# Performance work log

Hardware: AMD Instinct MI355X
Metric: run time of the kernel (lower is better)

The kernel has to match this reference:

```python
import jax, jax.numpy as jnp
import numpy as np

EMB = 384
HID = 256
HEADS = 4
HD = HID // HEADS  # 64
LAYERS = 2
M_DOCS = 32
TOTAL = 4096  # 1 query + 32 docs + 4063 sentences
LN_EPS = 1e-5


def _layernorm(x, scale, bias):
    mu = jnp.mean(x, axis=-1, keepdims=True)
    var = jnp.mean(jnp.square(x - mu), axis=-1, keepdims=True)
    return (x - mu) * jax.lax.rsqrt(var + LN_EPS) * scale + bias


def setup_inputs() -> dict:
    key = jax.random.key(0)
    ks = jax.random.split(key, 12)
    g = 0.05  # small init scale (stand-in for xavier)
    return {
        "node_embeddings": jax.random.normal(ks[0], (TOTAL, EMB), jnp.float32),
        "adj": jax.random.randint(ks[1], (TOTAL, TOTAL), 0, 2, jnp.int32),
        "num_docs": M_DOCS,
        "proj_w": jax.random.normal(ks[2], (HID, EMB), jnp.float32) * g,
        "proj_b": jnp.zeros((HID,), jnp.float32),
        "ln_scale": jnp.ones((LAYERS, HID), jnp.float32),
        "ln_bias": jnp.zeros((LAYERS, HID), jnp.float32),
        "gat_W": jax.random.normal(ks[3], (LAYERS, HEADS, HD, HID), jnp.float32) * g,
        "gat_a": jax.random.normal(ks[4], (LAYERS, HEADS, 2 * HD), jnp.float32) * g,
        "fusion_w": jax.random.normal(ks[5], (HID, 2 * HID + 2), jnp.float32) * g,
        "fusion_b": jnp.zeros((HID,), jnp.float32),
        "out_w": jax.random.normal(ks[6], (HID,), jnp.float32) * g,
        "out_b": jnp.float32(0.5),
    }


def reference(node_embeddings, adj, num_docs, proj_w, proj_b, ln_scale, ln_bias,
              gat_W, gat_a, fusion_w, fusion_b, out_w, out_b):
    T = node_embeddings.shape[0]
    M = num_docs
    N = T - 1 - M  # number of sentences
    # input projection + relu (dropout = identity in eval)
    h = jax.nn.relu(node_embeddings @ proj_w.T + proj_b)  # (T, HID)
    # query-guided sentence re-weighting
    q = h[0:1]                     # (1, HID)
    s = h[1 + M:]                  # (N, HID)
    qn = q / (jnp.linalg.norm(q, axis=1, keepdims=True) + 1e-8)
    sn = s / (jnp.linalg.norm(s, axis=1, keepdims=True) + 1e-8)
    cos = (qn @ sn.T).reshape(-1, 1)          # (N,1)
    s = s + 0.8 * q * cos
    h = jnp.concatenate([h[:1 + M], s], axis=0)
    mask = (adj == 0)[None]                   # (1,T,T)
    for i in range(LAYERS):
        res = h
        x = _layernorm(h, ln_scale[i], ln_bias[i])
        Wh = jnp.einsum('nd,hkd->hnk', x, gat_W[i])                # (H,T,HD)
        # concat-attention a.[Wh_i ; Wh_j] == a_src.Wh_i + a_dst.Wh_j
        src = jnp.einsum('hnk,hk->hn', Wh, gat_a[i, :, :HD])       # (H,T)
        dst = jnp.einsum('hnk,hk->hn', Wh, gat_a[i, :, HD:])       # (H,T)
        e = jax.nn.leaky_relu(src[:, :, None] + dst[:, None, :], 0.2)  # (H,T,T)
        e = jnp.where(mask, -jnp.inf, e)
        attn = jax.nn.softmax(e, axis=-1)                          # softmax over j
        hn = jnp.einsum('hij,hjk->hik', attn, Wh)                  # (H,T,HD)
        hcat = jnp.transpose(hn, (1, 0, 2)).reshape(T, HEADS * HD)
        h = 0.5 * jax.nn.relu(hcat) + 0.5 * res
    qh = h[0:1]
    sh = h[1 + M:]
    scores = (qh @ sh.T) / (HID ** 0.5)       # (1,N)
    aw = jax.nn.softmax(scores, axis=-1)
    awT = aw.T                                # (N,1)
    qw = qh * (awT + 0.5)                     # (N,HID)
    qnf = qh / (jnp.linalg.norm(qh, axis=1, keepdims=True) + 1e-8)
    snf = sh / (jnp.linalg.norm(sh, axis=1, keepdims=True) + 1e-8)
    cosf = (qnf @ snf.T).reshape(-1, 1)       # (N,1)
    feat = jnp.concatenate([sh, qw, cosf, awT], axis=1)  # (N, 2*HID+2)
    g = jax.nn.relu(feat @ fusion_w.T + fusion_b)
    out = g @ out_w + out_b                   # (N,)
    return out + 0.5 * cosf[:, 0]
```

## Files before the change

### kernel.cpp

```cpp
#include <hip/hip_runtime.h>
#include <hip/hip_bf16.h>
#include <stdint.h>

#define TOTAL 4096
#define EMB 384
#define MD 32
#define NDOCS (TOTAL - 1 - MD)
#define LN_EPS 1e-5f
#define NEGF (-1e30f)

typedef __hip_bfloat16 bf16;
typedef unsigned short ushort_t;
typedef __attribute__((ext_vector_type(8))) short short8;
typedef __attribute__((ext_vector_type(4))) float f32x4;
typedef __attribute__((ext_vector_type(2))) float f32x2;

__device__ __forceinline__ float ldf(const void* p, int i, int isbf) {
    return isbf ? __bfloat162float(((const bf16*)p)[i]) : ((const float*)p)[i];
}

__device__ __forceinline__ unsigned f2bf(float x) {
    return (__float_as_uint(x) + 0x8000u) >> 16;
}

__device__ __forceinline__ unsigned fenc(float f) {
    unsigned u = __float_as_uint(f);
    return (u >> 31) ? ~u : (u | 0x80000000u);
}
__device__ __forceinline__ float fdec(unsigned k) {
    return __uint_as_float((k & 0x80000000u) ? (k & 0x7FFFFFFFu) : ~k);
}

#define NTRANS ((EMB * 256 + 2 * 65536 + 514 * 256) / 256)
__global__ void k_adjmask(const int* adj, unsigned long long* maskb,
                          const uint16_t* embp, int* flag, unsigned* dmaxu,
                          const void* proj_w, const void* gat_W, const void* fusion_w,
                          float* projT, float* gatT, float* fwT) {
    __shared__ int red[4];
    int i = blockIdx.x, t = threadIdx.x;
    int w = t >> 6, l = t & 63;
    for (int c = w; c < 64; c += 4) {
        int a = adj[(size_t)i * TOTAL + c * 64 + l];
        unsigned long long m = __ballot(a != 0);
        if (l == 0) maskb[i * 64 + c] = m;
    }
    if (i == 0) {
        for (int idx = t; idx < 2048; idx += 256) dmaxu[idx] = 0x007FFFFFu;
    }
    if (i < NTRANS) {
        int cnt = 0;
        for (int k = t; k < 4096; k += 256) {
            uint16_t wd = embp[2 * k];
            int e = (wd >> 7) & 0xFF;
            if (e >= 100 && e <= 140) cnt++;
        }
        for (int o = 32; o > 0; o >>= 1) cnt += __shfl_down(cnt, o);
        if ((t & 63) == 0) red[t >> 6] = cnt;
        __syncthreads();
        int isbf = (red[0] + red[1] + red[2] + red[3] > 2048) ? 1 : 0;
        if (i == 0 && t == 0) flag[0] = isbf;
        int idx = i * 256 + t;
        if (idx < EMB * 256) {
            int d = idx >> 8, c = idx & 255;
            projT[idx] = ldf(proj_w, c * EMB + d, isbf);
        } else if (idx < EMB * 256 + 2 * 65536) {
            int r = idx - EMB * 256;
            int ll = r >> 16, rem = r & 65535;
            int d = rem >> 8, c = rem & 255;
            gatT[r] = ldf(gat_W, ll * 65536 + c * 256 + d, isbf);
        } else {
            int r = idx - (EMB * 256 + 2 * 65536);
            int j = r >> 8, c = r & 255;
            fwT[r] = ldf(fusion_w, c * 514 + j, isbf);
        }
    }
}

#define LR 8
__global__ __launch_bounds__(512) void k_lnwh(
        const void* emb, const void* proj_b, const float* projT,
        float* h, const float* gatT, const void* ln_scale, const void* ln_bias,
        const void* gat_a, ushort_t* whswz, float* srcb, unsigned* d12g,
        unsigned* dmaxu, int layer, const int* flagp) {
    __shared__ float embs[9][EMB];
    __shared__ float xs[8][256];
    __shared__ float red[2][LR][4];
    __shared__ float qred[4];
    int isbf = flagp[0];
    int t5 = threadIdx.x;
    int t = t5 & 255, half = t5 >> 8;
    int l = t5 & 63;
    int wh = (t5 >> 6) & 3;
    int i0 = blockIdx.x * LR;
    float hv[4];
    if (layer == 0) {
        for (int idx = t5; idx < 9 * EMB; idx += 512) {
            int r = idx / EMB, d = idx % EMB;
            embs[r][d] = ldf(emb, ((r < 8) ? (i0 + r) : 0) * EMB + d, isbf);
        }
        __syncthreads();
        float bias0 = ldf(proj_b, t, isbf);
        float acc[4] = {0.f, 0.f, 0.f, 0.f};
        float qacc = 0.f;
        for (int d0 = 0; d0 < EMB; d0 += 4) {
            float w0 = projT[d0 * 256 + t];
            float w1 = projT[(d0 + 1) * 256 + t];
            float w2 = projT[(d0 + 2) * 256 + t];
            float w3 = projT[(d0 + 3) * 256 + t];
            float4 xq = *(const float4*)&embs[8][d0];
            qacc = fmaf(xq.x, w0, qacc); qacc = fmaf(xq.y, w1, qacc);
            qacc = fmaf(xq.z, w2, qacc); qacc = fmaf(xq.w, w3, qacc);
#pragma unroll
            for (int r = 0; r < 4; r++) {
                float4 x = *(const float4*)&embs[half * 4 + r][d0];
                acc[r] = fmaf(x.x, w0, acc[r]); acc[r] = fmaf(x.y, w1, acc[r]);
                acc[r] = fmaf(x.z, w2, acc[r]); acc[r] = fmaf(x.w, w3, acc[r]);
            }
        }
        float qv = fmaxf(qacc + bias0, 0.f);
#pragma unroll
        for (int r = 0; r < 4; r++) hv[r] = fmaxf(acc[r] + bias0, 0.f);
        {
            float a = qv * qv;
            for (int o = 32; o > 0; o >>= 1) a += __shfl_down(a, o);
            if (half == 0 && l == 0) qred[wh] = a;
        }
#pragma unroll
        for (int r = 0; r < 4; r++) {
            float b = hv[r] * hv[r], c = qv * hv[r];
            for (int o = 32; o > 0; o >>= 1) { b += __shfl_down(b, o); c += __shfl_down(c, o); }
            if (l == 0) { red[0][half * 4 + r][wh] = b; red[1][half * 4 + r][wh] = c; }
        }
        __syncthreads();
        if (i0 + LR > 1 + MD) {
            float qn = sqrtf(qred[0] + qred[1] + qred[2] + qred[3]) + 1e-8f;
#pragma unroll
            for (int r = 0; r < 4; r++) {
                int rr = half * 4 + r;
                int i = i0 + rr;
                if (i >= 1 + MD) {
                    float bs = red[0][rr][0] + red[0][rr][1] + red[0][rr][2] + red[0][rr][3];
                    float cs = red[1][rr][0] + red[1][rr][1] + red[1][rr][2] + red[1][rr][3];
                    float k = 0.8f * (cs / (qn * (sqrtf(bs) + 1e-8f)));
                    hv[r] += k * qv;
                }
            }
        }
#pragma unroll
        for (int r = 0; r < 4; r++)
            h[(size_t)(i0 + half * 4 + r) * 256 + t] = hv[r];
        __syncthreads();
    } else {
#pragma unroll
        for (int r = 0; r < 4; r++)
            hv[r] = h[(size_t)(i0 + half * 4 + r) * 256 + t];
    }
    float scale = ldf(ln_scale, layer * 256 + t, isbf);
    float lbias = ldf(ln_bias, layer * 256 + t, isbf);
#pragma unroll
    for (int r = 0; r < 4; r++) {
        float a = hv[r], b = hv[r] * hv[r];
        for (int o = 32; o > 0; o >>= 1) { a += __shfl_down(a, o); b += __shfl_down(b, o); }
        if (l == 0) { red[0][half * 4 + r][wh] = a; red[1][half * 4 + r][wh] = b; }
    }
    __syncthreads();
#pragma unroll
    for (int r = 0; r < 4; r++) {
        int rr = half * 4 + r;
        float mu = (red[0][rr][0] + red[0][rr][1] + red[0][rr][2] + red[0][rr][3]) * (1.f / 256.f);
        float var = (red[1][rr][0] + red[1][rr][1] + red[1][rr][2] + red[1][rr][3]) * (1.f / 256.f) - mu * mu;
        xs[rr][t] = (hv[r] - mu) * rsqrtf(var + LN_EPS) * scale + lbias;
    }
    __syncthreads();
    const float* gT = gatT + layer * 65536;
    float acc2[4] = {0.f, 0.f, 0.f, 0.f};
    for (int d0 = 0; d0 < 256; d0 += 4) {
        float w0 = gT[d0 * 256 + t];
        float w1 = gT[(d0 + 1) * 256 + t];
        float w2 = gT[(d0 + 2) * 256 + t];
        float w3 = gT[(d0 + 3) * 256 + t];
#pragma unroll
        for (int r = 0; r < 4; r++) {
            float4 x = *(const float4*)&xs[half * 4 + r][d0];
            acc2[r] = fmaf(x.x, w0, acc2[r]); acc2[r] = fmaf(x.y, w1, acc2[r]);
            acc2[r] = fmaf(x.z, w2, acc2[r]); acc2[r] = fmaf(x.w, w3, acc2[r]);
        }
    }
    float av1 = ldf(gat_a, layer * 512 + wh * 128 + l, isbf);
    float av2 = ldf(gat_a, layer * 512 + wh * 128 + 64 + l, isbf);
    const float LOG2E = 1.44269504f;
    float mmax = -__builtin_inff();
#pragma unroll
    for (int r = 0; r < 4; r++) {
        int i = i0 + half * 4 + r;
        int off = (i >> 6) * 16384 + (t >> 6) * 4096 + ((i >> 3) & 7) * 512 +
                  ((t >> 4) & 3) * 128 + (t & 15) * 8 + (i & 7);
        whswz[off] = (ushort_t)f2bf(acc2[r]);
        float sv = acc2[r] * av1, dv = acc2[r] * av2;
        for (int o = 32; o > 0; o >>= 1) { sv += __shfl_down(sv, o); dv += __shfl_down(dv, o); }
        if (l == 0) {
            srcb[wh * 4096 + i] = sv;
            float D1 = exp2f(dv * LOG2E), D2 = exp2f(0.2f * dv * LOG2E);
            d12g[wh * 4096 + i] = (f2bf(D2) << 16) | f2bf(D1);
            mmax = fmaxf(mmax, dv);
        }
    }
    if (l == 0) atomicMax(&dmaxu[(blockIdx.x & 63) * 16 + wh], fenc(mmax));
}

#define TI 16
__global__ __launch_bounds__(512) void k_pv(const ushort_t* whswz, const float* srcb,
                                            const unsigned* dmaxu, const unsigned* d12g,
                                            const unsigned long long* maskb, float* h) {
    __shared__ unsigned long long mbs[16 * 66];
    __shared__ __align__(16) f32x4 accsh[16 * 64];
    __shared__ __align__(16) float lsh[4][4][4];
    __shared__ float srcs[64];
    __shared__ float dmx[4];
    __shared__ unsigned mlut[4];
    int t = threadIdx.x;
    int W = t >> 6, lane = t & 63;
    int hH = W & 3, kq = W >> 2;
    int quad = lane >> 4, c16 = lane & 15;
    int i0 = blockIdx.x * TI;
    if (t < 4) mlut[t] = (t & 1 ? 0x0000FFFFu : 0u) | (t & 2 ? 0xFFFF0000u : 0u);
    if (t < 256) {
        int hh = t >> 6, sl = t & 63;
        float v = fdec(dmaxu[sl * 16 + hh]);
        for (int o = 32; o > 0; o >>= 1) v = fmaxf(v, __shfl_xor(v, o));
        if (sl == 0) dmx[hh] = v;
    }
    for (int idx = t; idx < 16 * 64; idx += 512) {
        int r = idx >> 6, wd = idx & 63;
        mbs[r * 66 + wd] = maskb[(size_t)(i0 + r) * 64 + wd];
    }
    if (t < 64) srcs[t] = srcb[(t >> 4) * 4096 + i0 + (t & 15)];
    __syncthreads();
    const float LOG2E = 1.44269504f;
    float dm = dmx[hH];
    float src = srcs[hH * 16 + c16];
    float sd = src + dm;
    float rce = -fmaxf(sd, 0.2f * sd);
    float E1 = exp2f((src + rce) * LOG2E);
    float E2 = exp2f((0.2f * src + rce) * LOG2E);
    f32x4 acc[4];
    f32x4 accl = (f32x4){0.f, 0.f, 0.f, 0.f};
#pragma unroll
    for (int ct = 0; ct < 4; ct++) acc[ct] = (f32x4){0.f, 0.f, 0.f, 0.f};
    uint4 onesu;
    unsigned os = (c16 == 0) ? 0x3F803F80u : 0u;
    onesu.x = os; onesu.y = os; onesu.z = os; onesu.w = os;
    short8 bfones = __builtin_bit_cast(short8, onesu);
    const uint4* g4 = (const uint4*)whswz;
    const uint4* d4 = (const uint4*)d12g;
    size_t b0 = (size_t)hH * 512 + (size_t)(kq * 4 + quad) * 64 + c16;
    int dbase = hH * 1024, d0i = kq * 8 + quad * 2;
    uint4 bn[4], dn0, dn1;
#pragma unroll
    for (int ct = 0; ct < 4; ct++) bn[ct] = g4[b0 + ct * 16];
    dn0 = d4[dbase + d0i]; dn1 = d4[dbase + d0i + 1];
    for (int step = 0; step < 64; step++) {
        uint4 bc[4];
#pragma unroll
        for (int ct = 0; ct < 4; ct++) bc[ct] = bn[ct];
        uint4 dc0 = dn0, dc1 = dn1;
        if (step < 63) {
            size_t bs = b0 + (size_t)(step + 1) * 2048;
#pragma unroll
            for (int ct = 0; ct < 4; ct++) bn[ct] = g4[bs + ct * 16];
            int di = dbase + (step + 1) * 16 + d0i;
            dn0 = d4[di]; dn1 = d4[di + 1];
        }
        unsigned mby = (unsigned)(mbs[c16 * 66 + step] >> (kq * 32 + quad * 8)) & 0xFFu;
        unsigned dw[8] = {dc0.x, dc0.y, dc0.z, dc0.w, dc1.x, dc1.y, dc1.z, dc1.w};
        unsigned pu[4];
#pragma unroll
        for (int q = 0; q < 4; q++) {
            unsigned a = dw[2 * q], b = dw[2 * q + 1];
            f32x2 D1 = (f32x2){__uint_as_float(a << 16), __uint_as_float(b << 16)};
            f32x2 D2 = (f32x2){__uint_as_float(a & 0xFFFF0000u), __uint_as_float(b & 0xFFFF0000u)};
            f32x2 v1 = D1 * E1;
            f32x2 v2 = D2 * E2;
            f32x2 m = __builtin_elementwise_max(v1, v2);
            unsigned v = ((__float_as_uint(m.x) + 0x8000u) >> 16) |
                         ((__float_as_uint(m.y) + 0x8000u) & 0xFFFF0000u);
            pu[q] = v & mlut[(mby >> (2 * q)) & 3u];
        }
        uint4 afu;
        afu.x = pu[0]; afu.y = pu[1]; afu.z = pu[2]; afu.w = pu[3];
        short8 af = __builtin_bit_cast(short8, afu);
#pragma unroll
        for (int ct = 0; ct < 4; ct++) {
            short8 bf = __builtin_bit_cast(short8, bc[ct]);
            acc[ct] = __builtin_amdgcn_mfma_f32_16x16x32_bf16(af, bf, acc[ct], 0, 0, 0);
        }
        accl = __builtin_amdgcn_mfma_f32_16x16x32_bf16(af, bfones, accl, 0, 0, 0);
    }
    __syncthreads();
    if (kq == 1) {
#pragma unroll
        for (int ct = 0; ct < 4; ct++)
            accsh[(hH * 4 + ct) * 64 + lane] = acc[ct];
        if (c16 == 0) *(f32x4*)&lsh[hH][quad][0] = accl;
    }
    __syncthreads();
    if (kq == 0) {
        float ls[4];
#pragma unroll
        for (int rr = 0; rr < 4; rr++)
            ls[rr] = __shfl(accl[rr], quad * 16) + lsh[hH][quad][rr];
#pragma unroll
        for (int ct = 0; ct < 4; ct++) {
            f32x4 o = acc[ct] + accsh[(hH * 4 + ct) * 64 + lane];
#pragma unroll
            for (int rr = 0; rr < 4; rr++) {
                int row = i0 + quad * 4 + rr;
                size_t idx = (size_t)row * 256 + hH * 64 + ct * 16 + c16;
                float hn = 0.5f * fmaxf(o[rr] / ls[rr], 0.f) + 0.5f * h[idx];
                h[idx] = hn;
            }
        }
    }
}

__global__ __launch_bounds__(256) void k_scores(const float* h, float* scoresv, float* cosv,
                                                float* swp) {
    int t = threadIdx.x, W = t >> 6, lane = t & 63;
    const float4* h4 = (const float4*)h;
    int gw = blockIdx.x * 4 + W;
    float4 q4 = h4[lane];
    float a = q4.x * q4.x + q4.y * q4.y + q4.z * q4.z + q4.w * q4.w;
    for (int o = 32; o > 0; o >>= 1) a += __shfl_xor(a, o);
    float qn = sqrtf(a) + 1e-8f;
    float mw = NEGF, sw = 0.f;
    for (int n = gw; n < NDOCS; n += 1024) {
        float4 s4 = h4[(size_t)(1 + MD + n) * 64 + lane];
        float b = s4.x * s4.x + s4.y * s4.y + s4.z * s4.z + s4.w * s4.w;
        float c = q4.x * s4.x + q4.y * s4.y + q4.z * s4.z + q4.w * s4.w;
        for (int o = 32; o > 0; o >>= 1) { b += __shfl_xor(b, o); c += __shfl_xor(c, o); }
        float sc = c * (1.f / 16.f);
        if (lane == 0) {
            scoresv[n] = sc;
            cosv[n] = c / (qn * (sqrtf(b) + 1e-8f));
        }
        float mn = fmaxf(mw, sc);
        sw = sw * __expf(mw - mn) + __expf(sc - mn);
        mw = mn;
    }
    if (lane == 0) { swp[2 * gw] = mw; swp[2 * gw + 1] = sw; }
}

#define TN 8
__global__ __launch_bounds__(256) void k_fusion(const float* h,
                                                const float* scoresv, const float* swp,
                                                const float* cosv,
                                                const float* fwT, const void* fusion_b,
                                                const void* out_w, const void* out_bp,
                                                void* outv, const int* flagp) {
    __shared__ float feats2[514][TN];
    __shared__ float qhs[256];
    __shared__ float red[TN][4];
    __shared__ float reds[2][4];
    __shared__ float aws[TN];
    int isbf = flagp[0];
    int t = threadIdx.x;
    int n0 = blockIdx.x * TN;
    qhs[t] = h[t];
    float M = NEGF, S = 0.f;
    for (int idx = t; idx < 1024; idx += 256) {
        float pm = swp[2 * idx], ps = swp[2 * idx + 1];
        float mn = fmaxf(M, pm);
        S = S * __expf(M - mn) + ps * __expf(pm - mn);
        M = mn;
    }
    for (int o = 32; o > 0; o >>= 1) {
        float m2 = __shfl_xor(M, o), s2 = __shfl_xor(S, o);
        float mn = fmaxf(M, m2);
        S = S * __expf(M - mn) + s2 * __expf(m2 - mn);
        M = mn;
    }
    if ((t & 63) == 0) { reds[0][t >> 6] = M; reds[1][t >> 6] = S; }
    __syncthreads();
    float Mf = fmaxf(fmaxf(reds[0][0], reds[0][1]), fmaxf(reds[0][2], reds[0][3]));
    float Sf = reds[1][0] * __expf(reds[0][0] - Mf) + reds[1][1] * __expf(reds[0][1] - Mf) +
               reds[1][2] * __expf(reds[0][2] - Mf) + reds[1][3] * __expf(reds[0][3] - Mf);
    float invS = 1.f / Sf;
    if (t < TN) {
        int n = n0 + t;
        aws[t] = (n < NDOCS) ? __expf(scoresv[n] - Mf) * invS : 0.f;
    }
    __syncthreads();
    for (int idx = t; idx < 514 * TN; idx += 256) {
        int j = idx >> 3, r = idx & 7;
        int n = n0 + r;
        float v = 0.f;
        if (n < NDOCS) {
            if (j < 256) v = h[(size_t)(1 + MD + n) * 256 + j];
            else if (j < 512) v = qhs[j - 256] * (aws[r] + 0.5f);
            else if (j == 512) v = cosv[n];
            else v = aws[r];
        }
        feats2[j][r] = v;
    }
    __syncthreads();
    float acc[TN];
    float bk = ldf(fusion_b, t, isbf);
#pragma unroll
    for (int r = 0; r < TN; r++) acc[r] = bk;
    for (int j0 = 0; j0 < 512; j0 += 8) {
        float wv[8];
#pragma unroll
        for (int u = 0; u < 8; u++) wv[u] = fwT[(j0 + u) * 256 + t];
#pragma unroll
        for (int u = 0; u < 8; u++) {
            float4 fa = *(const float4*)&feats2[j0 + u][0];
            float4 fb = *(const float4*)&feats2[j0 + u][4];
            acc[0] = fmaf(fa.x, wv[u], acc[0]); acc[1] = fmaf(fa.y, wv[u], acc[1]);
            acc[2] = fmaf(fa.z, wv[u], acc[2]); acc[3] = fmaf(fa.w, wv[u], acc[3]);
            acc[4] = fmaf(fb.x, wv[u], acc[4]); acc[5] = fmaf(fb.y, wv[u], acc[5]);
            acc[6] = fmaf(fb.z, wv[u], acc[6]); acc[7] = fmaf(fb.w, wv[u], acc[7]);
        }
    }
#pragma unroll
    for (int j = 512; j < 514; j++) {
        float wv = fwT[j * 256 + t];
#pragma unroll
        for (int r = 0; r < TN; r++) acc[r] = fmaf(feats2[j][r], wv, acc[r]);
    }
    float ow = ldf(out_w, t, isbf);
    float outb = ldf(out_bp, 0, isbf);
#pragma unroll
    for (int r = 0; r < TN; r++) {
        float o = fmaxf(acc[r], 0.f) * ow;
        for (int off = 32; off > 0; off >>= 1) o += __shfl_down(o, off);
        if ((t & 63) == 0) red[r][t >> 6] = o;
    }
    __syncthreads();
    if (t < TN) {
        int n = n0 + t;
        if (n < NDOCS) {
            float o = red[t][0] + red[t][1] + red[t][2] + red[t][3] + outb + 0.5f * cosv[n];
            if (isbf) ((bf16*)outv)[n] = __float2bfloat16(o);
            else      ((float*)outv)[n] = o;
        }
    }
}

extern "C" void kernel_launch(void* const* d_in, const int* in_sizes, int n_in,
                              void* d_out, int out_size, void* d_ws, size_t ws_size,
                              hipStream_t stream) {
    const void* emb      = d_in[0];
    const int*  adj      = (const int*)d_in[1];
    const void* proj_w   = d_in[3];
    const void* proj_b   = d_in[4];
    const void* ln_scale = d_in[5];
    const void* ln_bias  = d_in[6];
    const void* gat_W    = d_in[7];
    const void* gat_a    = d_in[8];
    const void* fusion_w = d_in[9];
    const void* fusion_b = d_in[10];
    const void* out_w    = d_in[11];
    const void* out_b    = d_in[12];

    unsigned long long* maskb = (unsigned long long*)d_ws;
    int* flag = (int*)((char*)d_ws + (size_t)4096 * 64 * 8);
    float* f = (float*)((char*)d_ws + (size_t)4096 * 64 * 8 + 256);
    float* h       = f; f += 4096 * 256;
    float* srcb    = f; f += 4 * 4096;
    unsigned* d12g = (unsigned*)f; f += 4 * 4096;
    unsigned* dmaxu = (unsigned*)f; f += 2048;
    float* projT   = f; f += EMB * 256;
    float* gatT    = f; f += 2 * 65536;
    float* fwT     = f; f += 514 * 256;
    float* scoresv = f; f += 4096;
    float* cosv    = f; f += 4096;
    float* swpart  = f; f += 2048;
    ushort_t* whswz = (ushort_t*)f; f += 4096 * 256 / 2;

    k_adjmask<<<dim3(4096), dim3(256), 0, stream>>>(adj, maskb, (const uint16_t*)emb, flag,
                                                    dmaxu, proj_w, gat_W, fusion_w,
                                                    projT, gatT, fwT);
    for (int layer = 0; layer < 2; layer++) {
        k_lnwh<<<dim3(TOTAL / LR), dim3(512), 0, stream>>>(emb, proj_b, projT, h, gatT,
                                                           ln_scale, ln_bias, gat_a,
                                                           whswz, srcb, d12g,
                                                           dmaxu + layer * 1024, layer, flag);
        k_pv<<<dim3(TOTAL / TI), dim3(512), 0, stream>>>(whswz, srcb, dmaxu + layer * 1024,
                                                         d12g, maskb, h);
    }
    k_scores<<<dim3(256), dim3(256), 0, stream>>>(h, scoresv, cosv, swpart);
    k_fusion<<<dim3((NDOCS + TN - 1) / TN), dim3(256), 0, stream>>>(h, scoresv, swpart,
                                                                    cosv, fwT, fusion_b, out_w,
                                                                    out_b, (void*)d_out, flag);
}
```

Before: 317.8 us.

## Interleave transposed weights for float4 loads and deepen PV prefetch pipeline

The transposed projection, GAT and fusion weight layouts are reorganised so each thread reads four consecutive k-values as one float4, and the dense matvec loops software-prefetch the next weight vector. The attention PV kernel's register prefetch goes from one step ahead to two, using two alternating register sets. These aim to cut global load instruction count and hide memory latency, at the cost of more register pressure in the MFMA loop. fwT grows slightly to hold the padded 4-wide layout.

```diff
diff --git a/kernel.cpp b/kernel.cpp
--- a/kernel.cpp
+++ b/kernel.cpp
@@ -62,16 +62,17 @@
         int idx = i * 256 + t;
         if (idx < EMB * 256) {
             int d = idx >> 8, c = idx & 255;
-            projT[idx] = ldf(proj_w, c * EMB + d, isbf);
+            projT[(d >> 2) * 1024 + c * 4 + (d & 3)] = ldf(proj_w, c * EMB + d, isbf);
         } else if (idx < EMB * 256 + 2 * 65536) {
             int r = idx - EMB * 256;
             int ll = r >> 16, rem = r & 65535;
             int d = rem >> 8, c = rem & 255;
-            gatT[r] = ldf(gat_W, ll * 65536 + c * 256 + d, isbf);
+            gatT[ll * 65536 + (d >> 2) * 1024 + c * 4 + (d & 3)] =
+                ldf(gat_W, ll * 65536 + c * 256 + d, isbf);
         } else {
             int r = idx - (EMB * 256 + 2 * 65536);
             int j = r >> 8, c = r & 255;
-            fwT[r] = ldf(fusion_w, c * 514 + j, isbf);
+            fwT[(j >> 2) * 1024 + c * 4 + (j & 3)] = ldf(fusion_w, c * 514 + j, isbf);
         }
     }
 }
@@ -100,22 +101,23 @@
         }
         __syncthreads();
         float bias0 = ldf(proj_b, t, isbf);
+        const float4* pT4 = (const float4*)projT;
         float acc[4] = {0.f, 0.f, 0.f, 0.f};
         float qacc = 0.f;
-        for (int d0 = 0; d0 < EMB; d0 += 4) {
-            float w0 = projT[d0 * 256 + t];
-            float w1 = projT[(d0 + 1) * 256 + t];
-            float w2 = projT[(d0 + 2) * 256 + t];
-            float w3 = projT[(d0 + 3) * 256 + t];
+        float4 wc = pT4[t];
+        for (int k4 = 0; k4 < 96; k4++) {
+            float4 wn = pT4[(k4 < 95 ? k4 + 1 : 95) * 256 + t];
+            int d0 = k4 * 4;
             float4 xq = *(const float4*)&embs[8][d0];
-            qacc = fmaf(xq.x, w0, qacc); qacc = fmaf(xq.y, w1, qacc);
-            qacc = fmaf(xq.z, w2, qacc); qacc = fmaf(xq.w, w3, qacc);
+            qacc = fmaf(xq.x, wc.x, qacc); qacc = fmaf(xq.y, wc.y, qacc);
+            qacc = fmaf(xq.z, wc.z, qacc); qacc = fmaf(xq.w, wc.w, qacc);
 #pragma unroll
             for (int r = 0; r < 4; r++) {
                 float4 x = *(const float4*)&embs[half * 4 + r][d0];
-                acc[r] = fmaf(x.x, w0, acc[r]); acc[r] = fmaf(x.y, w1, acc[r]);
-                acc[r] = fmaf(x.z, w2, acc[r]); acc[r] = fmaf(x.w, w3, acc[r]);
+                acc[r] = fmaf(x.x, wc.x, acc[r]); acc[r] = fmaf(x.y, wc.y, acc[r]);
+                acc[r] = fmaf(x.z, wc.z, acc[r]); acc[r] = fmaf(x.w, wc.w, acc[r]);
             }
+            wc = wn;
         }
         float qv = fmaxf(qacc + bias0, 0.f);
 #pragma unroll
@@ -172,19 +174,19 @@
         xs[rr][t] = (hv[r] - mu) * rsqrtf(var + LN_EPS) * scale + lbias;
     }
     __syncthreads();
-    const float* gT = gatT + layer * 65536;
+    const float4* gT4 = (const float4*)(gatT + layer * 65536);
     float acc2[4] = {0.f, 0.f, 0.f, 0.f};
-    for (int d0 = 0; d0 < 256; d0 += 4) {
-        float w0 = gT[d0 * 256 + t];
-        float w1 = gT[(d0 + 1) * 256 + t];
-        float w2 = gT[(d0 + 2) * 256 + t];
-        float w3 = gT[(d0 + 3) * 256 + t];
+    float4 wc2 = gT4[t];
+    for (int k4 = 0; k4 < 64; k4++) {
+        float4 wn = gT4[(k4 < 63 ? k4 + 1 : 63) * 256 + t];
+        int d0 = k4 * 4;
 #pragma unroll
         for (int r = 0; r < 4; r++) {
             float4 x = *(const float4*)&xs[half * 4 + r][d0];
-            acc2[r] = fmaf(x.x, w0, acc2[r]); acc2[r] = fmaf(x.y, w1, acc2[r]);
-            acc2[r] = fmaf(x.z, w2, acc2[r]); acc2[r] = fmaf(x.w, w3, acc2[r]);
-        }
+            acc2[r] = fmaf(x.x, wc2.x, acc2[r]); acc2[r] = fmaf(x.y, wc2.y, acc2[r]);
+            acc2[r] = fmaf(x.z, wc2.z, acc2[r]); acc2[r] = fmaf(x.w, wc2.w, acc2[r]);
+        }
+        wc2 = wn;
     }
     float av1 = ldf(gat_a, layer * 512 + wh * 128 + l, isbf);
     float av2 = ldf(gat_a, layer * 512 + wh * 128 + 64 + l, isbf);
@@ -255,23 +257,21 @@
     const uint4* d4 = (const uint4*)d12g;
     size_t b0 = (size_t)hH * 512 + (size_t)(kq * 4 + quad) * 64 + c16;
     int dbase = hH * 1024, d0i = kq * 8 + quad * 2;
-    uint4 bn[4], dn0, dn1;
-#pragma unroll
-    for (int ct = 0; ct < 4; ct++) bn[ct] = g4[b0 + ct * 16];
-    dn0 = d4[dbase + d0i]; dn1 = d4[dbase + d0i + 1];
-    for (int step = 0; step < 64; step++) {
-        uint4 bc[4];
-#pragma unroll
-        for (int ct = 0; ct < 4; ct++) bc[ct] = bn[ct];
-        uint4 dc0 = dn0, dc1 = dn1;
-        if (step < 63) {
-            size_t bs = b0 + (size_t)(step + 1) * 2048;
-#pragma unroll
-            for (int ct = 0; ct < 4; ct++) bn[ct] = g4[bs + ct * 16];
-            int di = dbase + (step + 1) * 16 + d0i;
-            dn0 = d4[di]; dn1 = d4[di + 1];
-        }
-        unsigned mby = (unsigned)(mbs[c16 * 66 + step] >> (kq * 32 + quad * 8)) & 0xFFu;
+    uint4 bA0 = g4[b0],        bA1 = g4[b0 + 16],        bA2 = g4[b0 + 32],        bA3 = g4[b0 + 48];
+    uint4 bB0 = g4[b0 + 2048], bB1 = g4[b0 + 2048 + 16], bB2 = g4[b0 + 2048 + 32], bB3 = g4[b0 + 2048 + 48];
+    uint4 dA0 = d4[dbase + d0i],      dA1 = d4[dbase + d0i + 1];
+    uint4 dB0 = d4[dbase + 16 + d0i], dB1 = d4[dbase + 16 + d0i + 1];
+    auto pvstep = [&](uint4& B0, uint4& B1, uint4& B2, uint4& B3,
+                      uint4& DD0, uint4& DD1, int s) {
+        uint4 bc0 = B0, bc1 = B1, bc2 = B2, bc3 = B3;
+        uint4 dc0 = DD0, dc1 = DD1;
+        if (s < 62) {
+            size_t bs = b0 + (size_t)(s + 2) * 2048;
+            B0 = g4[bs]; B1 = g4[bs + 16]; B2 = g4[bs + 32]; B3 = g4[bs + 48];
+            int di = dbase + (s + 2) * 16 + d0i;
+            DD0 = d4[di]; DD1 = d4[di + 1];
+        }
+        unsigned mby = (unsigned)(mbs[c16 * 66 + s] >> (kq * 32 + quad * 8)) & 0xFFu;
         unsigned dw[8] = {dc0.x, dc0.y, dc0.z, dc0.w, dc1.x, dc1.y, dc1.z, dc1.w};
         unsigned pu[4];
 #pragma unroll
@@ -289,12 +289,15 @@
         uint4 afu;
         afu.x = pu[0]; afu.y = pu[1]; afu.z = pu[2]; afu.w = pu[3];
         short8 af = __builtin_bit_cast(short8, afu);
-#pragma unroll
-        for (int ct = 0; ct < 4; ct++) {
-            short8 bf = __builtin_bit_cast(short8, bc[ct]);
-            acc[ct] = __builtin_amdgcn_mfma_f32_16x16x32_bf16(af, bf, acc[ct], 0, 0, 0);
-        }
+        acc[0] = __builtin_amdgcn_mfma_f32_16x16x32_bf16(af, __builtin_bit_cast(short8, bc0), acc[0], 0, 0, 0);
+        acc[1] = __builtin_amdgcn_mfma_f32_16x16x32_bf16(af, __builtin_bit_cast(short8, bc1), acc[1], 0, 0, 0);
+        acc[2] = __builtin_amdgcn_mfma_f32_16x16x32_bf16(af, __builtin_bit_cast(short8, bc2), acc[2], 0, 0, 0);
+        acc[3] = __builtin_amdgcn_mfma_f32_16x16x32_bf16(af, __builtin_bit_cast(short8, bc3), acc[3], 0, 0, 0);
         accl = __builtin_amdgcn_mfma_f32_16x16x32_bf16(af, bfones, accl, 0, 0, 0);
+    };
+    for (int sp = 0; sp < 32; sp++) {
+        pvstep(bA0, bA1, bA2, bA3, dA0, dA1, 2 * sp);
+        pvstep(bB0, bB1, bB2, bB3, dB0, dB1, 2 * sp + 1);
     }
     __syncthreads();
     if (kq == 1) {
@@ -407,10 +410,11 @@
     float bk = ldf(fusion_b, t, isbf);
 #pragma unroll
     for (int r = 0; r < TN; r++) acc[r] = bk;
+    const float4* fT4 = (const float4*)fwT;
     for (int j0 = 0; j0 < 512; j0 += 8) {
-        float wv[8];
-#pragma unroll
-        for (int u = 0; u < 8; u++) wv[u] = fwT[(j0 + u) * 256 + t];
+        float4 wa = fT4[(j0 >> 2) * 256 + t];
+        float4 wb = fT4[((j0 >> 2) + 1) * 256 + t];
+        float wv[8] = {wa.x, wa.y, wa.z, wa.w, wb.x, wb.y, wb.z, wb.w};
 #pragma unroll
         for (int u = 0; u < 8; u++) {
             float4 fa = *(const float4*)&feats2[j0 + u][0];
@@ -421,11 +425,12 @@
             acc[6] = fmaf(fb.z, wv[u], acc[6]); acc[7] = fmaf(fb.w, wv[u], acc[7]);
         }
     }
-#pragma unroll
-    for (int j = 512; j < 514; j++) {
-        float wv = fwT[j * 256 + t];
-#pragma unroll
-        for (int r = 0; r < TN; r++) acc[r] = fmaf(feats2[j][r], wv, acc[r]);
+    {
+        float4 wt = fT4[128 * 256 + t];
+#pragma unroll
+        for (int r = 0; r < TN; r++) acc[r] = fmaf(feats2[512][r], wt.x, acc[r]);
+#pragma unroll
+        for (int r = 0; r < TN; r++) acc[r] = fmaf(feats2[513][r], wt.y, acc[r]);
     }
     float ow = ldf(out_w, t, isbf);
     float outb = ldf(out_bp, 0, isbf);
@@ -471,7 +476,7 @@
     unsigned* dmaxu = (unsigned*)f; f += 2048;
     float* projT   = f; f += EMB * 256;
     float* gatT    = f; f += 2 * 65536;
-    float* fwT     = f; f += 514 * 256;
+    float* fwT     = f; f += 129 * 1024;
     float* scoresv = f; f += 4096;
     float* cosv    = f; f += 4096;
     float* swpart  = f; f += 2048;
```

Measured after the change: 321.9 us. About the same (+1.3%).
